# Performance work log

Hardware: AMD Instinct MI355X
Metric: run time of the kernel (lower is better)

Reference implementation:

```python
import jax, jax.numpy as jnp
import numpy as np

N = 100000
IN_DIM = 128
HID = 64
OUT = 4


def _gcn_conv(x, W, b, src, dst, deg_inv_sqrt):
    """PyG GCNConv: linear transform, then symmetric-normalized scatter-add.
    src/dst already include self-loops; deg_inv_sqrt precomputed over them."""
    h = x @ W                                   # [N, H]
    norm = deg_inv_sqrt[src] * deg_inv_sqrt[dst]  # [E+N]
    msg = h[src] * norm[:, None]                # gather + scale, [E+N, H]
    out = jax.ops.segment_sum(msg, dst, num_segments=N)  # scatter-add
    return out + b


def setup_inputs() -> dict:
    key = jax.random.key(0)
    ks = jax.random.split(key, 8)
    E = 1600000
    x = jax.random.normal(ks[0], (N, IN_DIM), dtype=jnp.float32)
    edge_index = jax.random.randint(ks[1], (2, E), 0, N, dtype=jnp.int32)
    # Glorot-ish init for weights
    W1 = jax.random.normal(ks[2], (IN_DIM, HID), dtype=jnp.float32) / np.sqrt(IN_DIM)
    b1 = jnp.zeros((HID,), dtype=jnp.float32)
    W2 = jax.random.normal(ks[3], (HID, HID), dtype=jnp.float32) / np.sqrt(HID)
    b2 = jnp.zeros((HID,), dtype=jnp.float32)
    Wfc = jax.random.normal(ks[4], (HID, OUT), dtype=jnp.float32) / np.sqrt(HID)
    bfc = jnp.zeros((OUT,), dtype=jnp.float32)
    return {"x": x, "edge_index": edge_index, "W1": W1, "b1": b1,
            "W2": W2, "b2": b2, "Wfc": Wfc, "bfc": bfc}


def reference(x, edge_index, W1, b1, W2, b2, Wfc, bfc):
    # Add self-loops (GCNConv default add_self_loops=True)
    loops = jnp.arange(N, dtype=edge_index.dtype)
    src = jnp.concatenate([edge_index[0], loops])
    dst = jnp.concatenate([edge_index[1], loops])
    # Symmetric normalization: deg computed at aggregation targets (dst)
    deg = jax.ops.segment_sum(jnp.ones_like(dst, dtype=x.dtype), dst,
                              num_segments=N)
    deg_inv_sqrt = jnp.where(deg > 0, jax.lax.rsqrt(deg), 0.0)

    h = _gcn_conv(x, W1, b1, src, dst, deg_inv_sqrt)
    h = jax.nn.relu(h)                 # dropout is identity in eval mode
    h = _gcn_conv(h, W2, b2, src, dst, deg_inv_sqrt)
    h = jax.nn.relu(h)
    return h @ Wfc + bfc               # [N, 4]
```

## Files before the change

### kernel.cpp

```cpp
#include <hip/hip_runtime.h>
#include <hip/hip_fp16.h>


#define BCAP 5120
#define BINB 512
#define CHUNK 3200
#define CAP  64
#define LCAP 32

typedef float v2f __attribute__((ext_vector_type(2)));
typedef _Float16 f16x8 __attribute__((ext_vector_type(8)));
typedef float f32x4 __attribute__((ext_vector_type(4)));

__global__ __launch_bounds__(256) void k_bin_gemm1(
        const int* __restrict__ src, const int* __restrict__ dst, int e,
        int* bcur, unsigned* __restrict__ binned,
        const float* __restrict__ X, const float* __restrict__ W1,
        __half* __restrict__ Hh, int n) {
    __shared__ union {
        struct {
            unsigned ec[CHUNK];
            unsigned short eb[CHUNK];
            int lh[512], lbase[512], lr[512];
        } b;
        struct {
            _Float16 As[128 * 136];
            _Float16 Bs[64 * 136];
        } g;
    } sm;

    int t = threadIdx.x;

    if (blockIdx.x < BINB) {
        unsigned* ec = sm.b.ec;
        unsigned short* eb = sm.b.eb;
        int* lh = sm.b.lh; int* lbase = sm.b.lbase; int* lr = sm.b.lr;
        for (int i = t; i < 512; i += 256) { lh[i] = 0; lr[i] = 0; }
        __syncthreads();
        int chunk = (e + BINB - 1) / BINB;
        int lo = blockIdx.x * chunk;
        int hi = min(e, lo + chunk);
        for (int i = lo + t; i < hi; i += 256) {
            int d = dst[i];
            int b = d >> 8;
            ec[i - lo] = ((unsigned)src[i] << 8) | (unsigned)(d & 255);
            eb[i - lo] = (unsigned short)b;
            atomicAdd(&lh[b], 1);
        }
        __syncthreads();
        for (int i = t; i < 512; i += 256)
            lbase[i] = lh[i] ? atomicAdd(&bcur[i], lh[i]) : 0;
        __syncthreads();
        int cnt = hi - lo;
        for (int i = t; i < cnt; i += 256) {
            int b = eb[i];
            int r = lbase[b] + atomicAdd(&lr[b], 1);
            if (r < BCAP)
                binned[(size_t)b * BCAP + r] = ec[i];
        }
    } else {
        constexpr int K = 128, KP = 136;
        _Float16* As = sm.g.As;
        _Float16* Bs = sm.g.Bs;
        _Float16* H = (_Float16*)Hh;

        #pragma unroll
        for (int p = 0; p < 8; ++p) {
            int i = t + p * 256;
            int k = i >> 4, nn4 = (i & 15) << 2;
            float4 v = ((const float4*)W1)[i];
            Bs[(nn4 + 0) * KP + k] = (_Float16)v.x;
            Bs[(nn4 + 1) * KP + k] = (_Float16)v.y;
            Bs[(nn4 + 2) * KP + k] = (_Float16)v.z;
            Bs[(nn4 + 3) * KP + k] = (_Float16)v.w;
        }

        int row0 = (blockIdx.x - BINB) * 128;
        #pragma unroll
        for (int p = 0; p < 8; ++p) {
            int gi  = t + p * 256;
            int row = gi >> 4, sg = gi & 15;
            int grow = row0 + row;
            float4 v0 = make_float4(0.f, 0.f, 0.f, 0.f), v1 = v0;
            if (grow < n) {
                v0 = *(const float4*)(X + (size_t)grow * K + sg * 8);
                v1 = *(const float4*)(X + (size_t)grow * K + sg * 8 + 4);
            }
            union { __half2 h[4]; float4 f; } u;
            u.h[0] = __floats2half2_rn(v0.x, v0.y);
            u.h[1] = __floats2half2_rn(v0.z, v0.w);
            u.h[2] = __floats2half2_rn(v1.x, v1.y);
            u.h[3] = __floats2half2_rn(v1.z, v1.w);
            *(float4*)(As + row * KP + sg * 8) = u.f;
        }
        __syncthreads();

        int wv   = t >> 6;
        int lane = t & 63;
        int m    = lane & 15;
        int quad = lane >> 4;
        int r0   = wv * 32;

        f32x4 acc[2][4] = {};
        #pragma unroll
        for (int kb = 0; kb < K / 32; ++kb) {
            f16x8 af0 = *(const f16x8*)(As + (r0 + m) * KP + quad * 8 + kb * 32);
            f16x8 af1 = *(const f16x8*)(As + (r0 + 16 + m) * KP + quad * 8 + kb * 32);
            #pragma unroll
            for (int nt = 0; nt < 4; ++nt) {
                f16x8 bf = *(const f16x8*)(Bs + (nt * 16 + m) * KP + quad * 8 + kb * 32);
                acc[0][nt] = __builtin_amdgcn_mfma_f32_16x16x32_f16(af0, bf, acc[0][nt], 0, 0, 0);
                acc[1][nt] = __builtin_amdgcn_mfma_f32_16x16x32_f16(af1, bf, acc[1][nt], 0, 0, 0);
            }
        }

        #pragma unroll
        for (int mt = 0; mt < 2; ++mt) {
            int gr[4];
            #pragma unroll
            for (int r = 0; r < 4; ++r)
                gr[r] = row0 + r0 + mt * 16 + quad * 4 + r;
            #pragma unroll
            for (int nt = 0; nt < 4; ++nt)
                #pragma unroll
                for (int r = 0; r < 4; ++r) {
                    if (gr[r] < n)
                        H[(size_t)gr[r] * 64 + nt * 16 + m] =
                            (_Float16)acc[mt][nt][r];
                    else if (gr[r] == n)
                        H[(size_t)n * 64 + nt * 16 + m] = (_Float16)0.f;
                }
        }
    }
}

__global__ __launch_bounds__(256) void k_bucket2(const unsigned* __restrict__ binned,
                                                 const int* __restrict__ bcur,
                                                 int n, int* __restrict__ cnt,
                                                 int* __restrict__ slots) {
    __shared__ int lists[256 * (LCAP + 1)];
    __shared__ int lcnt[256];
    int b = blockIdx.x, t = threadIdx.x;
    int node0 = b << 8;
    size_t ebase = (size_t)b * BCAP;
    int ecnt = min(bcur[b], BCAP);
    lcnt[t] = 0;
    __syncthreads();
    for (int j = t; j < ecnt; j += 256) {
        unsigned ed = binned[ebase + j];
        int ld = ed & 255u;
        int s  = (int)(ed >> 8);
        int r  = atomicAdd(&lcnt[ld], 1);
        if (r < LCAP)
            lists[ld * (LCAP + 1) + r] = s;
        else if (r < CAP)
            slots[((size_t)(node0 + ld) << 6) + r] = s;
    }
    __syncthreads();
    int d = node0 + t;
    if (d < n) {
        int c = lcnt[t];
        cnt[d] = c;
        int m = min(c, LCAP);
        size_t base = (size_t)d << 6;
        for (int r = 0; r < m; ++r)
            slots[base + r] = lists[t * (LCAP + 1) + r];
    }
}

__global__ __launch_bounds__(256) void k_gemm2(const __half* __restrict__ X,
                                               const float* __restrict__ W2,
                                               const int* __restrict__ cnt,
                                               __half* __restrict__ Hh, int n) {
    constexpr int K = 64, KP = 72;
    __shared__ _Float16 As[128 * KP];
    __shared__ _Float16 Bs[64 * KP];

    int t = threadIdx.x;
    _Float16* H = (_Float16*)Hh;

    #pragma unroll
    for (int p = 0; p < 4; ++p) {
        int i = t + p * 256;
        int k = i >> 4, nn4 = (i & 15) << 2;
        float4 v = ((const float4*)W2)[i];
        Bs[(nn4 + 0) * KP + k] = (_Float16)v.x;
        Bs[(nn4 + 1) * KP + k] = (_Float16)v.y;
        Bs[(nn4 + 2) * KP + k] = (_Float16)v.z;
        Bs[(nn4 + 3) * KP + k] = (_Float16)v.w;
    }

    int row0 = blockIdx.x * 128;
    const __half* Xh = X;
    #pragma unroll
    for (int p = 0; p < 4; ++p) {
        int gi  = t + p * 256;
        int row = gi >> 3, sg = gi & 7;
        int grow = row0 + row;
        float4 v = make_float4(0.f, 0.f, 0.f, 0.f);
        if (grow < n)
            v = *(const float4*)(Xh + (size_t)grow * K + sg * 8);
        *(float4*)(As + row * KP + sg * 8) = v;
    }
    __syncthreads();

    int wv   = t >> 6;
    int lane = t & 63;
    int m    = lane & 15;
    int quad = lane >> 4;
    int r0   = wv * 32;

    f32x4 acc[2][4] = {};
    #pragma unroll
    for (int kb = 0; kb < K / 32; ++kb) {
        f16x8 af0 = *(const f16x8*)(As + (r0 + m) * KP + quad * 8 + kb * 32);
        f16x8 af1 = *(const f16x8*)(As + (r0 + 16 + m) * KP + quad * 8 + kb * 32);
        #pragma unroll
        for (int nt = 0; nt < 4; ++nt) {
            f16x8 bf = *(const f16x8*)(Bs + (nt * 16 + m) * KP + quad * 8 + kb * 32);
            acc[0][nt] = __builtin_amdgcn_mfma_f32_16x16x32_f16(af0, bf, acc[0][nt], 0, 0, 0);
            acc[1][nt] = __builtin_amdgcn_mfma_f32_16x16x32_f16(af1, bf, acc[1][nt], 0, 0, 0);
        }
    }

    #pragma unroll
    for (int mt = 0; mt < 2; ++mt) {
        float dv[4]; int gr[4];
        #pragma unroll
        for (int r = 0; r < 4; ++r) {
            gr[r] = row0 + r0 + mt * 16 + quad * 4 + r;
            dv[r] = (gr[r] < n) ? rsqrtf((float)(cnt[gr[r]] + 1)) : 0.f;
        }
        #pragma unroll
        for (int nt = 0; nt < 4; ++nt)
            #pragma unroll
            for (int r = 0; r < 4; ++r) {
                if (gr[r] < n)
                    H[(size_t)gr[r] * 64 + nt * 16 + m] =
                        (_Float16)(acc[mt][nt][r] * dv[r]);
                else if (gr[r] == n)
                    H[(size_t)n * 64 + nt * 16 + m] = (_Float16)0.f;
            }
    }
}

__device__ inline void add_row(const __half* __restrict__ hp, int s, int c4,
                               v2f& lo, v2f& hi) {
    float2 raw = *(const float2*)(hp + (size_t)s * 64 + c4);
    const __half2* p = (const __half2*)&raw;
    float2 l = __half22float2(p[0]);
    float2 h = __half22float2(p[1]);
    lo += (v2f){ l.x, l.y };
    hi += (v2f){ h.x, h.y };
}

__device__ inline void fma_row(const __half* __restrict__ hp, int s, int c4,
                               float w, v2f& lo, v2f& hi) {
    float2 raw = *(const float2*)(hp + (size_t)s * 64 + c4);
    const __half2* p = (const __half2*)&raw;
    float2 l = __half22float2(p[0]);
    float2 h = __half22float2(p[1]);
    lo += w * (v2f){ l.x, l.y };
    hi += w * (v2f){ h.x, h.y };
}

template<bool FUSE, bool SCALE>
__global__ __launch_bounds__(256) void k_gather(const __half* __restrict__ hp,
                                                const int* __restrict__ slots,
                                                const int* __restrict__ cnt,
                                                const float* __restrict__ bias,
                                                void* __restrict__ outb,
                                                const float* __restrict__ Wfc,
                                                const float* __restrict__ bfc,
                                                int n) {
    int lane = threadIdx.x & 63;
    int wid  = (blockIdx.x * blockDim.x + threadIdx.x) >> 6;
    if (wid >= n) return;
    int d    = wid;
    int esub = lane >> 4;
    int c4   = (lane & 15) * 4;

    size_t start = (size_t)d << 6;
    int num = cnt[d];
    int lim = min(num, CAP);
    int idx = (lane < lim) ? slots[start + lane] : 0;
    float dsv = 0.f;
    if constexpr (SCALE)
        dsv = rsqrtf((float)(cnt[idx] + 1));
    float dd = rsqrtf((float)(num + 1));

    v2f aL[4] = {}, aH[4] = {};
    if (esub == 0) {
        if constexpr (SCALE) fma_row(hp, d, c4, dd, aL[0], aH[0]);
        else                 add_row(hp, d, c4, aL[0], aH[0]);
    }

    int j = 0;
    for (; j + 16 <= lim; j += 16) {
        int s0 = __shfl(idx, j + esub);
        int s1 = __shfl(idx, j + 4 + esub);
        int s2 = __shfl(idx, j + 8 + esub);
        int s3 = __shfl(idx, j + 12 + esub);
        if constexpr (SCALE) {
            float w0 = __shfl(dsv, j + esub);
            float w1 = __shfl(dsv, j + 4 + esub);
            float w2 = __shfl(dsv, j + 8 + esub);
            float w3 = __shfl(dsv, j + 12 + esub);
            fma_row(hp, s0, c4, w0, aL[0], aH[0]);
            fma_row(hp, s1, c4, w1, aL[1], aH[1]);
            fma_row(hp, s2, c4, w2, aL[2], aH[2]);
            fma_row(hp, s3, c4, w3, aL[3], aH[3]);
        } else {
            add_row(hp, s0, c4, aL[0], aH[0]);
            add_row(hp, s1, c4, aL[1], aH[1]);
            add_row(hp, s2, c4, aL[2], aH[2]);
            add_row(hp, s3, c4, aL[3], aH[3]);
        }
    }
    for (; j < lim; j += 4) {
        int jj = j + esub;
        int sr = __shfl(idx, jj);
        int s  = (jj < lim) ? sr : n;
        if constexpr (SCALE) {
            float w = __shfl(dsv, jj);
            fma_row(hp, s, c4, w, aL[0], aH[0]);
        } else {
            add_row(hp, s, c4, aL[0], aH[0]);
        }
    }
    v2f sL = (aL[0] + aL[1]) + (aL[2] + aL[3]);
    v2f sH = (aH[0] + aH[1]) + (aH[2] + aH[3]);
    float4 a0 = make_float4(sL.x, sL.y, sH.x, sH.y);
    #pragma unroll
    for (int o = 16; o <= 32; o <<= 1) {
        a0.x += __shfl_xor(a0.x, o);
        a0.y += __shfl_xor(a0.y, o);
        a0.z += __shfl_xor(a0.z, o);
        a0.w += __shfl_xor(a0.w, o);
    }
    float4 bb = *(const float4*)(bias + c4);
    float4 o;
    o.x = fmaxf(bb.x + dd * a0.x, 0.f);
    o.y = fmaxf(bb.y + dd * a0.y, 0.f);
    o.z = fmaxf(bb.z + dd * a0.z, 0.f);
    o.w = fmaxf(bb.w + dd * a0.w, 0.f);
    if (!FUSE) {
        if (esub == 0) {
            union { __half2 h[2]; float2 f; } u;
            u.h[0] = __floats2half2_rn(o.x, o.y);
            u.h[1] = __floats2half2_rn(o.z, o.w);
            *(float2*)((__half*)outb + (size_t)d * 64 + c4) = u.f;
        }
    } else {
        const float4* W4 = (const float4*)Wfc;
        float4 w0 = W4[c4 + 0], w1 = W4[c4 + 1], w2 = W4[c4 + 2], w3 = W4[c4 + 3];
        float4 p;
        p.x = o.x * w0.x + o.y * w1.x + o.z * w2.x + o.w * w3.x;
        p.y = o.x * w0.y + o.y * w1.y + o.z * w2.y + o.w * w3.y;
        p.z = o.x * w0.z + o.y * w1.z + o.z * w2.z + o.w * w3.z;
        p.w = o.x * w0.w + o.y * w1.w + o.z * w2.w + o.w * w3.w;
        #pragma unroll
        for (int q = 1; q <= 8; q <<= 1) {
            p.x += __shfl_xor(p.x, q);
            p.y += __shfl_xor(p.y, q);
            p.z += __shfl_xor(p.z, q);
            p.w += __shfl_xor(p.w, q);
        }
        if (lane == 0) {
            float4 bf = *(const float4*)bfc;
            float4 r = make_float4(p.x + bf.x, p.y + bf.y, p.z + bf.z, p.w + bf.w);
            ((float4*)outb)[d] = r;
        }
    }
}

static inline size_t align256(size_t x) { return (x + 255) & ~(size_t)255; }

extern "C" void kernel_launch(void* const* d_in, const int* in_sizes, int n_in,
                              void* d_out, int out_size, void* d_ws, size_t ws_size,
                              hipStream_t stream) {
    const float* x   = (const float*)d_in[0];
    const int*   ei  = (const int*)d_in[1];
    const float* W1  = (const float*)d_in[2];
    const float* b1  = (const float*)d_in[3];
    const float* W2  = (const float*)d_in[4];
    const float* b2  = (const float*)d_in[5];
    const float* Wfc = (const float*)d_in[6];
    const float* bfc = (const float*)d_in[7];
    float* out = (float*)d_out;

    int n = in_sizes[0] / 128;
    int e = in_sizes[1] / 2;
    const int* src = ei;
    const int* dst = ei + e;

    char* ws = (char*)d_ws;
    size_t p = 0;
    int*      cnt    = (int*)     (ws + p); p = align256(p + (size_t)n * 4);
    int*      bcur   = (int*)     (ws + p); p = align256(p + 512 * 4);
    unsigned* binned = (unsigned*)(ws + p); p = align256(p + (size_t)512 * BCAP * 4);
    int*      slots  = (int*)     (ws + p); p = align256(p + (size_t)n * CAP * 4);
    __half*   hbuf   = (__half*)  (ws + p); p = align256(p + (size_t)(n + 1) * 64 * 2);
    __half*   a1h    = (__half*)  (ws + p);

    int gb  = (n + 127) / 128;
    int nbk = (n + 255) / 256;

    hipMemsetAsync(bcur, 0, 512 * sizeof(int), stream);
    k_bin_gemm1<<<BINB + gb, 256, 0, stream>>>(src, dst, e, bcur, binned,
                                               x, W1, hbuf, n);
    k_bucket2<<<nbk, 256, 0, stream>>>(binned, bcur, n, cnt, slots);

    k_gather<false, true><<<(n * 64 + 255) / 256, 256, 0, stream>>>(
        hbuf, slots, cnt, b1, a1h, nullptr, nullptr, n);

    k_gemm2<<<gb, 256, 0, stream>>>(a1h, W2, cnt, hbuf, n);
    k_gather<true, false><<<(n * 64 + 255) / 256, 256, 0, stream>>>(
        hbuf, slots, cnt, b2, out, Wfc, bfc, n);
}
```

Baseline: 253.3 us.

## Double binning blocks, halve GEMM row tiles, and coalesce bucket slot writes

The binning phase now uses twice as many blocks with half-sized edge chunks. Both GEMMs shrink their row tile from 128 to 64 rows, so each wave does a single 16-row MFMA strip, which increases block count and lowers shared memory per block. The bucket kernel's final copy of per-node lists into global slots is changed from one thread per node looping over entries to a strided loop over all node-slot pairs, so consecutive threads write neighbouring addresses. The cost is more blocks and more global atomics on bcur, plus less B-fragment reuse per block in the GEMMs.

```diff
diff --git a/kernel.cpp b/kernel.cpp
--- a/kernel.cpp
+++ b/kernel.cpp
@@ -3,8 +3,8 @@
 
 
 #define BCAP 5120
-#define BINB 512
-#define CHUNK 3200
+#define BINB 1024
+#define CHUNK 1600
 #define CAP  64
 #define LCAP 32
 
@@ -24,18 +24,16 @@
             int lh[512], lbase[512], lr[512];
         } b;
         struct {
-            _Float16 As[128 * 136];
+            _Float16 As[64 * 136];
             _Float16 Bs[64 * 136];
         } g;
     } sm;
 
     int t = threadIdx.x;
 
-    if (blockIdx.x < BINB) {
-        unsigned* ec = sm.b.ec;
-        unsigned short* eb = sm.b.eb;
-        int* lh = sm.b.lh; int* lbase = sm.b.lbase; int* lr = sm.b.lr;
-        for (int i = t; i < 512; i += 256) { lh[i] = 0; lr[i] = 0; }
+    if ((int)blockIdx.x < BINB) {
+        auto& B = sm.b;
+        for (int i = t; i < 512; i += 256) { B.lh[i] = 0; B.lr[i] = 0; }
         __syncthreads();
         int chunk = (e + BINB - 1) / BINB;
         int lo = blockIdx.x * chunk;
@@ -43,20 +41,20 @@
         for (int i = lo + t; i < hi; i += 256) {
             int d = dst[i];
             int b = d >> 8;
-            ec[i - lo] = ((unsigned)src[i] << 8) | (unsigned)(d & 255);
-            eb[i - lo] = (unsigned short)b;
-            atomicAdd(&lh[b], 1);
+            B.ec[i - lo] = ((unsigned)src[i] << 8) | (unsigned)(d & 255);
+            B.eb[i - lo] = (unsigned short)b;
+            atomicAdd(&B.lh[b], 1);
         }
         __syncthreads();
         for (int i = t; i < 512; i += 256)
-            lbase[i] = lh[i] ? atomicAdd(&bcur[i], lh[i]) : 0;
+            B.lbase[i] = B.lh[i] ? atomicAdd(&bcur[i], B.lh[i]) : 0;
         __syncthreads();
         int cnt = hi - lo;
         for (int i = t; i < cnt; i += 256) {
-            int b = eb[i];
-            int r = lbase[b] + atomicAdd(&lr[b], 1);
+            int b = B.eb[i];
+            int r = B.lbase[b] + atomicAdd(&B.lr[b], 1);
             if (r < BCAP)
-                binned[(size_t)b * BCAP + r] = ec[i];
+                binned[(size_t)b * BCAP + r] = B.ec[i];
         }
     } else {
         constexpr int K = 128, KP = 136;
@@ -75,9 +73,9 @@
             Bs[(nn4 + 3) * KP + k] = (_Float16)v.w;
         }
 
-        int row0 = (blockIdx.x - BINB) * 128;
-        #pragma unroll
-        for (int p = 0; p < 8; ++p) {
+        int row0 = ((int)blockIdx.x - BINB) * 64;
+        #pragma unroll
+        for (int p = 0; p < 4; ++p) {
             int gi  = t + p * 256;
             int row = gi >> 4, sg = gi & 15;
             int grow = row0 + row;
@@ -99,38 +97,32 @@
         int lane = t & 63;
         int m    = lane & 15;
         int quad = lane >> 4;
-        int r0   = wv * 32;
-
-        f32x4 acc[2][4] = {};
+        int r0   = wv * 16;
+
+        f32x4 acc[4] = {};
         #pragma unroll
         for (int kb = 0; kb < K / 32; ++kb) {
-            f16x8 af0 = *(const f16x8*)(As + (r0 + m) * KP + quad * 8 + kb * 32);
-            f16x8 af1 = *(const f16x8*)(As + (r0 + 16 + m) * KP + quad * 8 + kb * 32);
+            f16x8 af = *(const f16x8*)(As + (r0 + m) * KP + quad * 8 + kb * 32);
             #pragma unroll
             for (int nt = 0; nt < 4; ++nt) {
                 f16x8 bf = *(const f16x8*)(Bs + (nt * 16 + m) * KP + quad * 8 + kb * 32);
-                acc[0][nt] = __builtin_amdgcn_mfma_f32_16x16x32_f16(af0, bf, acc[0][nt], 0, 0, 0);
-                acc[1][nt] = __builtin_amdgcn_mfma_f32_16x16x32_f16(af1, bf, acc[1][nt], 0, 0, 0);
+                acc[nt] = __builtin_amdgcn_mfma_f32_16x16x32_f16(af, bf, acc[nt], 0, 0, 0);
             }
         }
 
-        #pragma unroll
-        for (int mt = 0; mt < 2; ++mt) {
-            int gr[4];
+        int gr[4];
+        #pragma unroll
+        for (int r = 0; r < 4; ++r)
+            gr[r] = row0 + r0 + quad * 4 + r;
+        #pragma unroll
+        for (int nt = 0; nt < 4; ++nt)
             #pragma unroll
-            for (int r = 0; r < 4; ++r)
-                gr[r] = row0 + r0 + mt * 16 + quad * 4 + r;
-            #pragma unroll
-            for (int nt = 0; nt < 4; ++nt)
-                #pragma unroll
-                for (int r = 0; r < 4; ++r) {
-                    if (gr[r] < n)
-                        H[(size_t)gr[r] * 64 + nt * 16 + m] =
-                            (_Float16)acc[mt][nt][r];
-                    else if (gr[r] == n)
-                        H[(size_t)n * 64 + nt * 16 + m] = (_Float16)0.f;
-                }
-        }
+            for (int r = 0; r < 4; ++r) {
+                if (gr[r] < n)
+                    H[(size_t)gr[r] * 64 + nt * 16 + m] = (_Float16)acc[nt][r];
+                else if (gr[r] == n)
+                    H[(size_t)n * 64 + nt * 16 + m] = (_Float16)0.f;
+            }
     }
 }
 
@@ -157,14 +149,13 @@
             slots[((size_t)(node0 + ld) << 6) + r] = s;
     }
     __syncthreads();
-    int d = node0 + t;
-    if (d < n) {
-        int c = lcnt[t];
-        cnt[d] = c;
-        int m = min(c, LCAP);
-        size_t base = (size_t)d << 6;
-        for (int r = 0; r < m; ++r)
-            slots[base + r] = lists[t * (LCAP + 1) + r];
+    if (node0 + t < n) cnt[node0 + t] = lcnt[t];
+    for (int k = t; k < 256 * LCAP; k += 256) {
+        int ld = k >> 5;
+        int r  = k & (LCAP - 1);
+        if (r < min(lcnt[ld], LCAP) && node0 + ld < n)
+            slots[((size_t)(node0 + ld) << 6) + r] =
+                lists[ld * (LCAP + 1) + r];
     }
 }
 
@@ -173,7 +164,7 @@
                                                const int* __restrict__ cnt,
                                                __half* __restrict__ Hh, int n) {
     constexpr int K = 64, KP = 72;
-    __shared__ _Float16 As[128 * KP];
+    __shared__ _Float16 As[64 * KP];
     __shared__ _Float16 Bs[64 * KP];
 
     int t = threadIdx.x;
@@ -190,10 +181,10 @@
         Bs[(nn4 + 3) * KP + k] = (_Float16)v.w;
     }
 
-    int row0 = blockIdx.x * 128;
+    int row0 = blockIdx.x * 64;
     const __half* Xh = X;
     #pragma unroll
-    for (int p = 0; p < 4; ++p) {
+    for (int p = 0; p < 2; ++p) {
         int gi  = t + p * 256;
         int row = gi >> 3, sg = gi & 7;
         int grow = row0 + row;
@@ -208,40 +199,35 @@
     int lane = t & 63;
     int m    = lane & 15;
     int quad = lane >> 4;
-    int r0   = wv * 32;
-
-    f32x4 acc[2][4] = {};
+    int r0   = wv * 16;
+
+    f32x4 acc[4] = {};
     #pragma unroll
     for (int kb = 0; kb < K / 32; ++kb) {
-        f16x8 af0 = *(const f16x8*)(As + (r0 + m) * KP + quad * 8 + kb * 32);
-        f16x8 af1 = *(const f16x8*)(As + (r0 + 16 + m) * KP + quad * 8 + kb * 32);
+        f16x8 af = *(const f16x8*)(As + (r0 + m) * KP + quad * 8 + kb * 32);
         #pragma unroll
         for (int nt = 0; nt < 4; ++nt) {
             f16x8 bf = *(const f16x8*)(Bs + (nt * 16 + m) * KP + quad * 8 + kb * 32);
-            acc[0][nt] = __builtin_amdgcn_mfma_f32_16x16x32_f16(af0, bf, acc[0][nt], 0, 0, 0);
-            acc[1][nt] = __builtin_amdgcn_mfma_f32_16x16x32_f16(af1, bf, acc[1][nt], 0, 0, 0);
-        }
-    }
-
-    #pragma unroll
-    for (int mt = 0; mt < 2; ++mt) {
-        float dv[4]; int gr[4];
+            acc[nt] = __builtin_amdgcn_mfma_f32_16x16x32_f16(af, bf, acc[nt], 0, 0, 0);
+        }
+    }
+
+    float dv[4]; int gr[4];
+    #pragma unroll
+    for (int r = 0; r < 4; ++r) {
+        gr[r] = row0 + r0 + quad * 4 + r;
+        dv[r] = (gr[r] < n) ? rsqrtf((float)(cnt[gr[r]] + 1)) : 0.f;
+    }
+    #pragma unroll
+    for (int nt = 0; nt < 4; ++nt)
         #pragma unroll
         for (int r = 0; r < 4; ++r) {
-            gr[r] = row0 + r0 + mt * 16 + quad * 4 + r;
-            dv[r] = (gr[r] < n) ? rsqrtf((float)(cnt[gr[r]] + 1)) : 0.f;
-        }
-        #pragma unroll
-        for (int nt = 0; nt < 4; ++nt)
-            #pragma unroll
-            for (int r = 0; r < 4; ++r) {
-                if (gr[r] < n)
-                    H[(size_t)gr[r] * 64 + nt * 16 + m] =
-                        (_Float16)(acc[mt][nt][r] * dv[r]);
-                else if (gr[r] == n)
-                    H[(size_t)n * 64 + nt * 16 + m] = (_Float16)0.f;
-            }
-    }
+            if (gr[r] < n)
+                H[(size_t)gr[r] * 64 + nt * 16 + m] =
+                    (_Float16)(acc[nt][r] * dv[r]);
+            else if (gr[r] == n)
+                H[(size_t)n * 64 + nt * 16 + m] = (_Float16)0.f;
+        }
 }
 
 __device__ inline void add_row(const __half* __restrict__ hp, int s, int c4,
@@ -403,7 +389,7 @@
     __half*   hbuf   = (__half*)  (ws + p); p = align256(p + (size_t)(n + 1) * 64 * 2);
     __half*   a1h    = (__half*)  (ws + p);
 
-    int gb  = (n + 127) / 128;
+    int gb  = (n + 64) / 64;
     int nbk = (n + 255) / 256;
 
     hipMemsetAsync(bcur, 0, 512 * sizeof(int), stream);
```

Result: slower. 265.9 us (+4.9%).
